# Optimization experiments

Hardware: AMD Instinct MI355X
Metric: run time of the kernel (lower is better)

The kernel has to match this reference:

```python
import jax, jax.numpy as jnp
import numpy as np

NC = 80
CONF = 0.25
IOU_T = 0.45
MAX_DET = 100
ATTN_RES = 14
NUM_BASE = 5
TOPK = 1024          # candidate pre-filter (EfficientNMS-style)
SCALE = 0.25         # spatial_scale of ROIAlign


def setup_inputs() -> dict:
    key = jax.random.key(0)
    k1, k2, k3, k4 = jax.random.split(key, 4)
    B, A = 4, 25200
    test = jax.random.uniform(k1, (B, A, 5 + NC), dtype=jnp.float32)
    # scale boxes to image coords: cx,cy in [0,608), w,h in [0,120)
    box_scale = jnp.concatenate([jnp.array([608., 608., 120., 120.], jnp.float32),
                                 jnp.ones(1 + NC, jnp.float32)])
    test = test * box_scale
    attn = jax.random.normal(k2, (B, A, NUM_BASE * ATTN_RES * ATTN_RES), dtype=jnp.float32)
    bases = jax.random.normal(k3, (B, NUM_BASE - 1, 160, 160), dtype=jnp.float32)
    sem = jax.random.normal(k4, (B, 1, 160, 160), dtype=jnp.float32)
    return {"test": test, "attn": attn, "bases": bases, "sem": sem}


def _iou_matrix(b):
    # b: [K,4] xyxy
    area = jnp.clip(b[:, 2] - b[:, 0], 0) * jnp.clip(b[:, 3] - b[:, 1], 0)
    lt = jnp.maximum(b[:, None, :2], b[None, :, :2])
    rb = jnp.minimum(b[:, None, 2:], b[None, :, 2:])
    wh = jnp.clip(rb - lt, 0)
    inter = wh[..., 0] * wh[..., 1]
    return inter / (area[:, None] + area[None, :] - inter + 1e-9)


def _nms_single(boxes, scores):
    # boxes [A,4], scores [A,NC]. Class-aware greedy NMS over top-K candidates.
    flat = scores.reshape(-1)
    flat = jnp.where(flat > CONF, flat, -jnp.inf)
    top_s, top_i = jax.lax.top_k(flat, TOPK)
    anchor = top_i // NC
    cls = top_i % NC
    cb = boxes[anchor]                                   # [K,4]
    sup = (_iou_matrix(cb) > IOU_T) & (cls[:, None] == cls[None, :])

    def step(valid, _):
        s = jnp.where(valid, top_s, -jnp.inf)
        j = jnp.argmax(s)
        ok = jnp.isfinite(s[j])
        nv = (valid & ~sup[j]).at[j].set(False)
        return jnp.where(ok, nv, valid), (j, ok)

    _, (sel, selok) = jax.lax.scan(step, jnp.isfinite(top_s), None, length=MAX_DET)
    dboxes = jnp.where(selok[:, None], cb[sel], 0.)
    dscores = jnp.where(selok, top_s[sel], 0.)
    dcls = jnp.where(selok, cls[sel], 0).astype(jnp.int32)
    didx = jnp.where(selok, anchor[sel], 0).astype(jnp.int32)
    return selok.sum().astype(jnp.int32), dboxes, dscores, dcls, didx


def _roi_align(feat, rois, bidx, oh, ow, scale):
    # feat [B,C,H,W], rois [N,4] xyxy (input coords), half_pixel transform,
    # avg mode, 1 sample/bin (adaptive ratio = 1 here since bins < 1 px).
    N = rois.shape[0]
    B, C, H, W = feat.shape
    x1 = rois[:, 0] * scale - 0.5
    y1 = rois[:, 1] * scale - 0.5
    x2 = rois[:, 2] * scale - 0.5
    y2 = rois[:, 3] * scale - 0.5
    ys = y1[:, None] + (jnp.arange(oh, dtype=feat.dtype) + 0.5) * ((y2 - y1) / oh)[:, None]
    xs = x1[:, None] + (jnp.arange(ow, dtype=feat.dtype) + 0.5) * ((x2 - x1) / ow)[:, None]

    def axis(coord, dim):
        valid = (coord > -1.0) & (coord < dim)
        c = jnp.clip(coord, 0.0, dim - 1.0)
        lo = jnp.floor(c)
        hi = jnp.clip(lo + 1, 0, dim - 1)
        return lo.astype(jnp.int32), hi.astype(jnp.int32), c - lo, valid

    y0, y1i, wy, vy = axis(ys, H)
    x0, x1i, wx, vx = axis(xs, W)
    featn = feat[bidx]                                   # [N,C,H,W]
    n = jnp.arange(N)[:, None, None]

    def g(Y, X):  # -> [N,oh,ow,C]
        return featn[n, :, Y[:, :, None], X[:, None, :]]

    wy_ = wy[:, :, None, None]
    wx_ = wx[:, None, :, None]
    val = (g(y0, x0) * (1 - wy_) * (1 - wx_) + g(y0, x1i) * (1 - wy_) * wx_
           + g(y1i, x0) * wy_ * (1 - wx_) + g(y1i, x1i) * wy_ * wx_)
    val = jnp.where((vy[:, :, None] & vx[:, None, :])[..., None], val, 0.)
    return jnp.transpose(val, (0, 3, 1, 2))                # [N,C,oh,ow]


def _forward(test, attn, bases_in, sem):
    bases = jnp.concatenate([bases_in, sem], axis=1)       # [B,5,H,W]
    conv = jnp.array([[1, 0, 1, 0], [0, 1, 0, 1],
                      [-0.5, 0, 0.5, 0], [0, -0.5, 0, 0.5]], test.dtype)
    boxes = test[:, :, :4] @ conv                          # cxcywh -> xyxy
    scores = test[:, :, 5:5 + NC] * test[:, :, 4:5]
    _, dboxes, dscores, dcls, didx = jax.vmap(_nms_single)(boxes, scores)
    B, P, H, W = bases.shape
    bidx = jnp.repeat(jnp.arange(B), MAX_DET)              # [B*D]
    box_i = didx.reshape(-1)
    sel_boxes = boxes[bidx, box_i]                         # [N,4]
    sel_masks = attn[bidx, box_i]                          # [N,980]
    pooled = _roi_align(bases, sel_boxes, bidx, H, W, SCALE)  # [N,5,H,W]
    coeffs = sel_masks.reshape(-1, NUM_BASE, ATTN_RES, ATTN_RES)
    coeffs = jax.image.resize(coeffs, (coeffs.shape[0], NUM_BASE, H, W), 'linear')
    coeffs = jax.nn.softmax(coeffs, axis=1)
    masks = jax.nn.sigmoid((pooled * coeffs).sum(axis=1).reshape(B, MAX_DET, H * W))
    return jnp.concatenate([dboxes, dscores[..., None],
                            dcls.astype(test.dtype)[..., None], masks], axis=-1)


def reference(test, attn, bases, sem):
    return _forward(test, attn, bases, sem)
```

## Files before the change

### kernel.cpp

```cpp
#include <hip/hip_runtime.h>
#include <stdint.h>

#define B_   4
#define A_   25200
#define NC_  80
#define ROW_ 85
#define ATT_ 980
#define MAXDET_ 100
#define TOPK_ 1024
#define CAP_  4096
#define OUTSTRIDE_ 25606
#define HW_ 160
#define HWHW_ 25600
#define CONF_ 0.25f
#define IOUT_ 0.45f

#define WS_HIST 0
#define WS_CNT  4096
#define WS_TB   4160
#define WS_NTOP 4224
#define WS_CAND 8192
#define WS_TOPV 139264
#define WS_TOPA 155648
#define WS_TOPC 172032
#define WS_CB   188416
#define WS_SUP  253952
#define WS_DETA 778240

typedef unsigned long long u64;
typedef unsigned u32;

__global__ void k_clear(char* w) {
    int i = blockIdx.x * 256 + threadIdx.x;
    if (i < 1028) ((u32*)w)[i] = 0u;
}

__global__ void k_hist(const float* __restrict__ test, char* __restrict__ w) {
    int b = blockIdx.y;
    __shared__ u32 h[256];
    if (threadIdx.x < 256) h[threadIdx.x] = 0u;
    __syncthreads();
    const int total = A_ * NC_;
    for (int e = blockIdx.x * 256 + threadIdx.x; e < total; e += 128 * 256) {
        u32 a = (u32)e / 80u;
        u32 c = (u32)e - a * 80u;
        const float* row = test + ((size_t)b * A_ + a) * ROW_;
        float s = row[5 + c] * row[4];
        if (s > CONF_) {
            u32 key = __float_as_uint(s);
            int wb = (int)(key >> 17) - 7936;
            wb = wb < 0 ? 0 : (wb > 255 ? 255 : wb);
            atomicAdd(&h[wb], 1u);
        }
    }
    __syncthreads();
    u32* hist = (u32*)(w + WS_HIST);
    if (threadIdx.x < 256 && h[threadIdx.x]) atomicAdd(&hist[b * 256 + threadIdx.x], h[threadIdx.x]);
}

__global__ void k_thresh(char* w) {
    if (threadIdx.x < B_) {
        int b = threadIdx.x;
        const u32* h = (const u32*)(w + WS_HIST) + b * 256;
        u32 cum = 0; int wtb = 0;
        for (int i = 255; i >= 0; --i) {
            cum += h[i];
            if (cum >= TOPK_) { wtb = i; break; }
        }
        ((int*)(w + WS_TB))[b] = wtb;
    }
}

__global__ void k_collect(const float* __restrict__ test, char* __restrict__ w) {
    int b = blockIdx.y;
    int wtb = ((const int*)(w + WS_TB))[b];
    u32* cnt = (u32*)(w + WS_CNT);
    u64* cand = (u64*)(w + WS_CAND);
    const int total = A_ * NC_;
    for (int e = blockIdx.x * 256 + threadIdx.x; e < total; e += 128 * 256) {
        u32 a = (u32)e / 80u;
        u32 c = (u32)e - a * 80u;
        const float* row = test + ((size_t)b * A_ + a) * ROW_;
        float s = row[5 + c] * row[4];
        if (s > CONF_) {
            u32 key = __float_as_uint(s);
            int wb = (int)(key >> 17) - 7936;
            wb = wb < 0 ? 0 : (wb > 255 ? 255 : wb);
            if (wb >= wtb) {
                u32 pos = atomicAdd(&cnt[b], 1u);
                if (pos < CAP_)
                    cand[(size_t)b * CAP_ + pos] = ((u64)key << 32) | (u64)(0xFFFFFFFFu - (u32)e);
            }
        }
    }
}

__global__ __launch_bounds__(1024) void k_sort(const float* __restrict__ test, char* __restrict__ w) {
    int b = blockIdx.x;
    __shared__ u64 sm[CAP_];
    u32 cnt = ((const u32*)(w + WS_CNT))[b];
    int n = cnt < CAP_ ? (int)cnt : CAP_;
    const u64* cand = (const u64*)(w + WS_CAND) + (size_t)b * CAP_;
    for (int i = threadIdx.x; i < CAP_; i += 1024) sm[i] = (i < n) ? cand[i] : 0ull;
    __syncthreads();
    for (int k = 2; k <= CAP_; k <<= 1) {
        for (int j = k >> 1; j > 0; j >>= 1) {
            for (int t = threadIdx.x; t < CAP_; t += 1024) {
                int ixj = t ^ j;
                if (ixj > t) {
                    u64 a = sm[t], c = sm[ixj];
                    bool desc = ((t & k) == 0);
                    if (desc ? (a < c) : (a > c)) { sm[t] = c; sm[ixj] = a; }
                }
            }
            __syncthreads();
        }
    }
    int ntop = n < TOPK_ ? n : TOPK_;
    if (threadIdx.x == 0) ((int*)(w + WS_NTOP))[b] = ntop;
    if (threadIdx.x < TOPK_) {
        int i = threadIdx.x;
        float* topv = (float*)(w + WS_TOPV);
        int* topa = (int*)(w + WS_TOPA);
        int* topc = (int*)(w + WS_TOPC);
        float4* cb = (float4*)(w + WS_CB);
        if (i < ntop) {
            u64 v = sm[i];
            u32 key = (u32)(v >> 32);
            u32 idx = 0xFFFFFFFFu - (u32)(v & 0xFFFFFFFFull);
            u32 anchor = idx / 80u;
            u32 cls = idx - anchor * 80u;
            const float* tr = test + ((size_t)b * A_ + anchor) * ROW_;
            float cx = tr[0], cy = tr[1], ww = tr[2], hh = tr[3];
            float4 box;
            box.x = cx - 0.5f * ww; box.y = cy - 0.5f * hh;
            box.z = cx + 0.5f * ww; box.w = cy + 0.5f * hh;
            topv[b * TOPK_ + i] = __uint_as_float(key);
            topa[b * TOPK_ + i] = (int)anchor;
            topc[b * TOPK_ + i] = (int)cls;
            cb[b * TOPK_ + i] = box;
        } else {
            topv[b * TOPK_ + i] = 0.f;
            topa[b * TOPK_ + i] = 0;
            topc[b * TOPK_ + i] = 0;
            cb[b * TOPK_ + i] = make_float4(0.f, 0.f, 0.f, 0.f);
        }
    }
}

__device__ __forceinline__ bool sup_pair(float4 a, float4 b, int ca, int cbb) {
#pragma clang fp contract(off)
    if (ca != cbb) return false;
    float areaA = fmaxf(a.z - a.x, 0.f) * fmaxf(a.w - a.y, 0.f);
    float areaB = fmaxf(b.z - b.x, 0.f) * fmaxf(b.w - b.y, 0.f);
    float ltx = fmaxf(a.x, b.x), lty = fmaxf(a.y, b.y);
    float rbx = fminf(a.z, b.z), rby = fminf(a.w, b.w);
    float iw = fmaxf(rbx - ltx, 0.f), ih = fmaxf(rby - lty, 0.f);
    float inter = iw * ih;
    float iou = inter / (((areaA + areaB) - inter) + 1e-9f);
    return iou > IOUT_;
}

__global__ void k_sup(char* __restrict__ w) {
    int b = blockIdx.y;
    int t = blockIdx.x * 256 + threadIdx.x;
    int row = t >> 4, chunk = t & 15;
    const float4* cb = (const float4*)(w + WS_CB) + (size_t)b * TOPK_;
    const int* topc = (const int*)(w + WS_TOPC) + (size_t)b * TOPK_;
    float4 rb = cb[row];
    int rc = topc[row];
    u64 bits = 0ull;
    int base = chunk * 64;
    for (int cc = 0; cc < 64; ++cc) {
        if (sup_pair(rb, cb[base + cc], rc, topc[base + cc])) bits |= (1ull << cc);
    }
    ((u64*)(w + WS_SUP))[((size_t)b * TOPK_ + row) * 16 + chunk] = bits;
}

__global__ void k_nms(char* __restrict__ w, float* __restrict__ out) {
    int b = blockIdx.x;
    int lane = threadIdx.x;
    int ntop = ((const int*)(w + WS_NTOP))[b];
    const u64* sup = (const u64*)(w + WS_SUP);
    __shared__ int selA[MAXDET_];
    __shared__ int okA[MAXDET_];
    u32 valid = 0u;
    for (int t = 0; t < 16; ++t)
        if (lane * 16 + t < ntop) valid |= (1u << t);
    for (int k = 0; k < MAXDET_; ++k) {
        u64 bal = __ballot(valid != 0u);
        if (bal == 0ull) {
            if (lane == 0) { selA[k] = 0; okA[k] = 0; }
            continue;
        }
        int L = __ffsll(bal) - 1;
        u32 vL = (u32)__shfl((int)valid, L);
        int j = L * 16 + (__ffs(vL & 0xFFFFu) - 1);
        u64 chunk = sup[((size_t)b * TOPK_ + j) * 16 + (lane >> 2)];
        u32 s16 = (u32)(chunk >> ((lane & 3) * 16)) & 0xFFFFu;
        valid &= ~s16;
        if (lane == L) valid &= ~(1u << (j & 15));
        if (lane == 0) { selA[k] = j; okA[k] = 1; }
    }
    __syncthreads();
    const float* topv = (const float*)(w + WS_TOPV) + (size_t)b * TOPK_;
    const int* topa = (const int*)(w + WS_TOPA) + (size_t)b * TOPK_;
    const int* topc = (const int*)(w + WS_TOPC) + (size_t)b * TOPK_;
    const float4* cb = (const float4*)(w + WS_CB) + (size_t)b * TOPK_;
    int* deta = (int*)(w + WS_DETA);
    for (int k = lane; k < MAXDET_; k += 64) {
        int ok = okA[k], s = selA[k];
        float b0 = 0, b1 = 0, b2 = 0, b3 = 0, sc = 0; int cls_ = 0, anc = 0;
        if (ok) {
            float4 bb = cb[s];
            b0 = bb.x; b1 = bb.y; b2 = bb.z; b3 = bb.w;
            sc = topv[s]; cls_ = topc[s]; anc = topa[s];
        }
        size_t o = ((size_t)(b * MAXDET_ + k)) * OUTSTRIDE_;
        out[o + 0] = b0; out[o + 1] = b1; out[o + 2] = b2; out[o + 3] = b3;
        out[o + 4] = sc; out[o + 5] = (float)cls_;
        deta[b * MAXDET_ + k] = anc;
    }
}

__global__ void k_mask(const float* __restrict__ test, const float* __restrict__ attn,
                       const float* __restrict__ bases, const float* __restrict__ sem,
                       const char* __restrict__ w, float* __restrict__ out) {
    int roi = blockIdx.x;
    int b = roi / MAXDET_;
    int anchor = ((const int*)(w + WS_DETA))[roi];
    const float* t = test + ((size_t)b * A_ + anchor) * ROW_;
    float cx = t[0], cy = t[1], ww = t[2], hh = t[3];
    float bx1 = cx - 0.5f * ww, by1 = cy - 0.5f * hh;
    float bx2 = cx + 0.5f * ww, by2 = cy + 0.5f * hh;
    float rx1 = bx1 * 0.25f - 0.5f, ry1 = by1 * 0.25f - 0.5f;
    float rx2 = bx2 * 0.25f - 0.5f, ry2 = by2 * 0.25f - 0.5f;
    float xstep = (rx2 - rx1) / 160.f, ystep = (ry2 - ry1) / 160.f;

    __shared__ float att[5 * 196];
    __shared__ float sxw[HW_], syw[HW_], rzw[HW_];
    __shared__ int sxlo[HW_], sxhi[HW_], sylo[HW_], syhi[HW_];
    __shared__ int sxv[HW_], syv[HW_], rzlo[HW_];

    const float* arow = attn + ((size_t)b * A_ + anchor) * ATT_;
    for (int i = threadIdx.x; i < ATT_; i += 256) att[i] = arow[i];
    if (threadIdx.x < HW_) {
        int i = threadIdx.x;
        float coord = rx1 + (i + 0.5f) * xstep;
        sxv[i] = (coord > -1.0f) && (coord < 160.0f);
        float c = fminf(fmaxf(coord, 0.f), 159.f);
        float lo = floorf(c);
        sxlo[i] = (int)lo; sxhi[i] = min((int)lo + 1, 159); sxw[i] = c - lo;
        coord = ry1 + (i + 0.5f) * ystep;
        syv[i] = (coord > -1.0f) && (coord < 160.0f);
        c = fminf(fmaxf(coord, 0.f), 159.f);
        lo = floorf(c);
        sylo[i] = (int)lo; syhi[i] = min((int)lo + 1, 159); syw[i] = c - lo;
        float f = (i + 0.5f) * (14.f / 160.f) - 0.5f;
        float rc = fminf(fmaxf(f, 0.f), 13.f);
        float rlo = floorf(rc);
        rzlo[i] = (int)rlo; rzw[i] = rc - rlo;
    }
    __syncthreads();

    const float* bp[5];
    bp[0] = bases + ((size_t)b * 4 + 0) * HWHW_;
    bp[1] = bases + ((size_t)b * 4 + 1) * HWHW_;
    bp[2] = bases + ((size_t)b * 4 + 2) * HWHW_;
    bp[3] = bases + ((size_t)b * 4 + 3) * HWHW_;
    bp[4] = sem + (size_t)b * HWHW_;

    size_t obase = (size_t)roi * OUTSTRIDE_ + 6;
    int pstart = blockIdx.y * (HWHW_ / 8);
    int pend = pstart + (HWHW_ / 8);
    for (int p = pstart + (int)threadIdx.x; p < pend; p += 256) {
        int y = p / HW_, x = p - y * HW_;
        int ylo = sylo[y], yhi = syhi[y]; float wy = syw[y];
        int xlo = sxlo[x], xhi = sxhi[x]; float wx = sxw[x];
        bool v = sxv[x] && syv[y];
        float w00 = (1.f - wy) * (1.f - wx), w01 = (1.f - wy) * wx;
        float w10 = wy * (1.f - wx), w11 = wy * wx;
        int i00 = ylo * HW_ + xlo, i01 = ylo * HW_ + xhi;
        int i10 = yhi * HW_ + xlo, i11 = yhi * HW_ + xhi;
        float pooled[5];
#pragma unroll
        for (int c5 = 0; c5 < 5; ++c5) {
            float g = bp[c5][i00] * w00 + bp[c5][i01] * w01 + bp[c5][i10] * w10 + bp[c5][i11] * w11;
            pooled[c5] = v ? g : 0.f;
        }
        int cylo = rzlo[y]; float cwy = rzw[y]; int cyhi = min(cylo + 1, 13);
        int cxlo = rzlo[x]; float cwx = rzw[x]; int cxhi = min(cxlo + 1, 13);
        float c00 = (1.f - cwy) * (1.f - cwx), c01 = (1.f - cwy) * cwx;
        float c10 = cwy * (1.f - cwx), c11 = cwy * cwx;
        int j00 = cylo * 14 + cxlo, j01 = cylo * 14 + cxhi;
        int j10 = cyhi * 14 + cxlo, j11 = cyhi * 14 + cxhi;
        float cf[5]; float m = -1e30f;
#pragma unroll
        for (int c5 = 0; c5 < 5; ++c5) {
            const float* ap = att + c5 * 196;
            float g = ap[j00] * c00 + ap[j01] * c01 + ap[j10] * c10 + ap[j11] * c11;
            cf[c5] = g; m = fmaxf(m, g);
        }
        float se = 0.f, dot = 0.f;
#pragma unroll
        for (int c5 = 0; c5 < 5; ++c5) {
            float e = __expf(cf[c5] - m);
            se += e; dot += pooled[c5] * e;
        }
        dot /= se;
        out[obase + p] = 1.f / (1.f + __expf(-dot));
    }
}

extern "C" void kernel_launch(void* const* d_in, const int* in_sizes, int n_in,
                              void* d_out, int out_size, void* d_ws, size_t ws_size,
                              hipStream_t stream) {
    const float* test = (const float*)d_in[0];
    const float* attn = (const float*)d_in[1];
    const float* bases = (const float*)d_in[2];
    const float* sem = (const float*)d_in[3];
    float* out = (float*)d_out;
    char* w = (char*)d_ws;

    k_clear<<<5, 256, 0, stream>>>(w);
    k_hist<<<dim3(128, B_), 256, 0, stream>>>(test, w);
    k_thresh<<<1, 64, 0, stream>>>(w);
    k_collect<<<dim3(128, B_), 256, 0, stream>>>(test, w);
    k_sort<<<B_, 1024, 0, stream>>>(test, w);
    k_sup<<<dim3(64, B_), 256, 0, stream>>>(w);
    k_nms<<<B_, 64, 0, stream>>>(w, out);
    k_mask<<<dim3(B_ * MAXDET_, 8), 256, 0, stream>>>(test, attn, bases, sem, w, out);
}
```

Baseline: 711.9 us.

## Use separable bilinear interpolation with shared-memory row staging in mask kernel

```diff
diff --git a/kernel.cpp b/kernel.cpp
--- a/kernel.cpp
+++ b/kernel.cpp
@@ -223,10 +223,11 @@
     }
 }
 
-__global__ void k_mask(const float* __restrict__ test, const float* __restrict__ attn,
+__global__ __launch_bounds__(256) void k_mask(const float* __restrict__ test, const float* __restrict__ attn,
                        const float* __restrict__ bases, const float* __restrict__ sem,
                        const char* __restrict__ w, float* __restrict__ out) {
     int roi = blockIdx.x;
+    int by = blockIdx.y;
     int b = roi / MAXDET_;
     int anchor = ((const int*)(w + WS_DETA))[roi];
     const float* t = test + ((size_t)b * A_ + anchor) * ROW_;
@@ -237,31 +238,49 @@
     float rx2 = bx2 * 0.25f - 0.5f, ry2 = by2 * 0.25f - 0.5f;
     float xstep = (rx2 - rx1) / 160.f, ystep = (ry2 - ry1) / 160.f;
 
-    __shared__ float att[5 * 196];
-    __shared__ float sxw[HW_], syw[HW_], rzw[HW_];
-    __shared__ int sxlo[HW_], sxhi[HW_], sylo[HW_], syhi[HW_];
-    __shared__ int sxv[HW_], syv[HW_], rzlo[HW_];
-
+    __shared__ float XR[5 * 8 * 160];
+    __shared__ float CXR[5 * 4 * 160];
+    __shared__ float att[ATT_];
+    __shared__ int   sxlo[HW_], sxhi[HW_];
+    __shared__ float sxw[HW_], sxvF[HW_];
+    __shared__ int   rzlo[HW_];
+    __shared__ float rzw[HW_];
+    __shared__ int   yloA[20], yhiA[20], cyloA[20], cyhiA[20];
+    __shared__ float ywA[20], cwyA[20], yvF[20];
+    __shared__ int rminS, crminS;
+
+    int tid = threadIdx.x;
     const float* arow = attn + ((size_t)b * A_ + anchor) * ATT_;
-    for (int i = threadIdx.x; i < ATT_; i += 256) att[i] = arow[i];
-    if (threadIdx.x < HW_) {
-        int i = threadIdx.x;
-        float coord = rx1 + (i + 0.5f) * xstep;
-        sxv[i] = (coord > -1.0f) && (coord < 160.0f);
+    for (int i = tid; i < ATT_; i += 256) att[i] = arow[i];
+    if (tid < HW_) {
+        float coord = rx1 + (tid + 0.5f) * xstep;
+        sxvF[tid] = (coord > -1.0f && coord < 160.0f) ? 1.f : 0.f;
         float c = fminf(fmaxf(coord, 0.f), 159.f);
         float lo = floorf(c);
-        sxlo[i] = (int)lo; sxhi[i] = min((int)lo + 1, 159); sxw[i] = c - lo;
-        coord = ry1 + (i + 0.5f) * ystep;
-        syv[i] = (coord > -1.0f) && (coord < 160.0f);
-        c = fminf(fmaxf(coord, 0.f), 159.f);
-        lo = floorf(c);
-        sylo[i] = (int)lo; syhi[i] = min((int)lo + 1, 159); syw[i] = c - lo;
-        float f = (i + 0.5f) * (14.f / 160.f) - 0.5f;
+        sxlo[tid] = (int)lo; sxhi[tid] = min((int)lo + 1, 159); sxw[tid] = c - lo;
+        float f = (tid + 0.5f) * (14.f / 160.f) - 0.5f;
         float rc = fminf(fmaxf(f, 0.f), 13.f);
         float rlo = floorf(rc);
-        rzlo[i] = (int)rlo; rzw[i] = rc - rlo;
-    }
-    __syncthreads();
+        rzlo[tid] = (int)rlo; rzw[tid] = rc - rlo;
+    }
+    __syncthreads();
+    if (tid < 20) {
+        int yg = by * 20 + tid;
+        float coord = ry1 + (yg + 0.5f) * ystep;
+        yvF[tid] = (coord > -1.0f && coord < 160.0f) ? 1.f : 0.f;
+        float c = fminf(fmaxf(coord, 0.f), 159.f);
+        float lo = floorf(c);
+        yloA[tid] = (int)lo; yhiA[tid] = min((int)lo + 1, 159); ywA[tid] = c - lo;
+        cyloA[tid] = rzlo[yg]; cwyA[tid] = rzw[yg]; cyhiA[tid] = min(rzlo[yg] + 1, 13);
+    }
+    __syncthreads();
+    if (tid == 0) {
+        int rm = 159, cm = 13;
+        for (int i = 0; i < 20; ++i) { rm = min(rm, yloA[i]); cm = min(cm, cyloA[i]); }
+        rminS = rm; crminS = cm;
+    }
+    __syncthreads();
+    int rmin = rminS, crmin = crminS;
 
     const float* bp[5];
     bp[0] = bases + ((size_t)b * 4 + 0) * HWHW_;
@@ -270,45 +289,72 @@
     bp[3] = bases + ((size_t)b * 4 + 3) * HWHW_;
     bp[4] = sem + (size_t)b * HWHW_;
 
-    size_t obase = (size_t)roi * OUTSTRIDE_ + 6;
-    int pstart = blockIdx.y * (HWHW_ / 8);
-    int pend = pstart + (HWHW_ / 8);
-    for (int p = pstart + (int)threadIdx.x; p < pend; p += 256) {
-        int y = p / HW_, x = p - y * HW_;
-        int ylo = sylo[y], yhi = syhi[y]; float wy = syw[y];
-        int xlo = sxlo[x], xhi = sxhi[x]; float wx = sxw[x];
-        bool v = sxv[x] && syv[y];
-        float w00 = (1.f - wy) * (1.f - wx), w01 = (1.f - wy) * wx;
-        float w10 = wy * (1.f - wx), w11 = wy * wx;
-        int i00 = ylo * HW_ + xlo, i01 = ylo * HW_ + xhi;
-        int i10 = yhi * HW_ + xlo, i11 = yhi * HW_ + xhi;
-        float pooled[5];
+    for (int idx = tid; idx < 5 * 8 * 160; idx += 256) {
+        int c = idx / (8 * 160);
+        int rem = idx - c * (8 * 160);
+        int r = rem / 160;
+        int x = rem - r * 160;
+        int row = min(rmin + r, 159);
+        const float* pb = bp[c] + row * 160;
+        float wx = sxw[x];
+        XR[idx] = pb[sxlo[x]] * (1.f - wx) + pb[sxhi[x]] * wx;
+    }
+    for (int idx = tid; idx < 5 * 4 * 160; idx += 256) {
+        int c = idx / (4 * 160);
+        int rem = idx - c * (4 * 160);
+        int rr = rem / 160;
+        int x = rem - rr * 160;
+        int row = min(crmin + rr, 13);
+        const float* pa = att + c * 196 + row * 14;
+        int xl = rzlo[x]; int xh = min(xl + 1, 13); float wxc = rzw[x];
+        CXR[idx] = pa[xl] * (1.f - wxc) + pa[xh] * wxc;
+    }
+    __syncthreads();
+
+    size_t obase = (size_t)roi * OUTSTRIDE_ + 6 + (size_t)by * 20 * HW_;
+    for (int g = tid; g < 800; g += 256) {
+        int yl = g / 40;
+        int x4 = (g - yl * 40) * 4;
+        float wy = ywA[yl], vy = yvF[yl], cwy = cwyA[yl];
+        int rlo = min(max(yloA[yl] - rmin, 0), 7);
+        int rhi = min(max(yhiA[yl] - rmin, 0), 7);
+        int clo = min(max(cyloA[yl] - crmin, 0), 3);
+        int chi = min(max(cyhiA[yl] - crmin, 0), 3);
+        float p4[5][4], cf4[5][4];
 #pragma unroll
-        for (int c5 = 0; c5 < 5; ++c5) {
-            float g = bp[c5][i00] * w00 + bp[c5][i01] * w01 + bp[c5][i10] * w10 + bp[c5][i11] * w11;
-            pooled[c5] = v ? g : 0.f;
-        }
-        int cylo = rzlo[y]; float cwy = rzw[y]; int cyhi = min(cylo + 1, 13);
-        int cxlo = rzlo[x]; float cwx = rzw[x]; int cxhi = min(cxlo + 1, 13);
-        float c00 = (1.f - cwy) * (1.f - cwx), c01 = (1.f - cwy) * cwx;
-        float c10 = cwy * (1.f - cwx), c11 = cwy * cwx;
-        int j00 = cylo * 14 + cxlo, j01 = cylo * 14 + cxhi;
-        int j10 = cyhi * 14 + cxlo, j11 = cyhi * 14 + cxhi;
-        float cf[5]; float m = -1e30f;
+        for (int c = 0; c < 5; ++c) {
+            float4 a = *(const float4*)&XR[(c * 8 + rlo) * 160 + x4];
+            float4 bq = *(const float4*)&XR[(c * 8 + rhi) * 160 + x4];
+            p4[c][0] = a.x * (1.f - wy) + bq.x * wy;
+            p4[c][1] = a.y * (1.f - wy) + bq.y * wy;
+            p4[c][2] = a.z * (1.f - wy) + bq.z * wy;
+            p4[c][3] = a.w * (1.f - wy) + bq.w * wy;
+            float4 ca = *(const float4*)&CXR[(c * 4 + clo) * 160 + x4];
+            float4 cbq = *(const float4*)&CXR[(c * 4 + chi) * 160 + x4];
+            cf4[c][0] = ca.x * (1.f - cwy) + cbq.x * cwy;
+            cf4[c][1] = ca.y * (1.f - cwy) + cbq.y * cwy;
+            cf4[c][2] = ca.z * (1.f - cwy) + cbq.z * cwy;
+            cf4[c][3] = ca.w * (1.f - cwy) + cbq.w * cwy;
+        }
+        float4 vx4 = *(const float4*)&sxvF[x4];
+        float vx[4] = { vx4.x, vx4.y, vx4.z, vx4.w };
+        float res[4];
 #pragma unroll
-        for (int c5 = 0; c5 < 5; ++c5) {
-            const float* ap = att + c5 * 196;
-            float g = ap[j00] * c00 + ap[j01] * c01 + ap[j10] * c10 + ap[j11] * c11;
-            cf[c5] = g; m = fmaxf(m, g);
-        }
-        float se = 0.f, dot = 0.f;
+        for (int i = 0; i < 4; ++i) {
+            float v = vx[i] * vy;
+            float se = 0.f, dot = 0.f;
 #pragma unroll
-        for (int c5 = 0; c5 < 5; ++c5) {
-            float e = __expf(cf[c5] - m);
-            se += e; dot += pooled[c5] * e;
-        }
-        dot /= se;
-        out[obase + p] = 1.f / (1.f + __expf(-dot));
+            for (int c = 0; c < 5; ++c) {
+                float e = __expf(cf4[c][i]);
+                se += e;
+                dot += p4[c][i] * e;
+            }
+            float r = v * dot / se;
+            res[i] = 1.f / (1.f + __expf(-r));
+        }
+        float2* o2 = (float2*)(out + obase + (size_t)yl * HW_ + x4);
+        o2[0] = make_float2(res[0], res[1]);
+        o2[1] = make_float2(res[2], res[3]);
     }
 }
 
```

After: 735.0 us. +3.2%, slower.
